# Kernel optimization log

Hardware: AMD Instinct MI355X
Metric: run time of the kernel (lower is better)

Reference implementation:

```python
import jax, jax.numpy as jnp
import numpy as np

N = 32000
E = 512000
IN_C = 16
OUT_C = 16
EDGE_DIM = 8
HID = 32


def setup_inputs() -> dict:
    key = jax.random.key(0)
    ks = jax.random.split(key, 8)
    x = jax.random.normal(ks[0], (N, IN_C), dtype=jnp.float32)
    edge_index = jax.random.randint(ks[1], (2, E), 0, N, dtype=jnp.int32)
    pseudo = jax.random.uniform(ks[2], (E, EDGE_DIM), dtype=jnp.float32)
    W1 = jax.random.normal(ks[3], (EDGE_DIM, HID), dtype=jnp.float32) * (1.0 / np.sqrt(EDGE_DIM))
    b1 = jnp.zeros((HID,), dtype=jnp.float32)
    W2 = jax.random.normal(ks[4], (HID, IN_C * OUT_C), dtype=jnp.float32) * (1.0 / np.sqrt(HID))
    b2 = jnp.zeros((IN_C * OUT_C,), dtype=jnp.float32)
    root = jax.random.normal(ks[5], (IN_C, OUT_C), dtype=jnp.float32) * (1.0 / np.sqrt(IN_C))
    bias = jnp.zeros((OUT_C,), dtype=jnp.float32)
    return {"x": x, "edge_index": edge_index, "pseudo": pseudo,
            "W1": W1, "b1": b1, "W2": W2, "b2": b2,
            "root": root, "bias": bias}


def reference(x, edge_index, pseudo, W1, b1, W2, b2, root, bias):
    row, col = edge_index[0], edge_index[1]
    # edge MLP h_Theta: [E, edge_dim] -> [E, in*out]
    h = jax.nn.relu(pseudo @ W1 + b1)
    w = (h @ W2 + b2).reshape(-1, IN_C, OUT_C)  # [E, in, out]
    # gather source features, per-edge matmul: [E, in] x [E, in, out] -> [E, out]
    msg = jnp.einsum('ei,eio->eo', x[col], w)
    # scatter-add messages to destination nodes (aggr='add')
    out = jax.ops.segment_sum(msg, row, num_segments=N)
    # root transform + bias
    out = out + x @ root + bias
    return out
```

## Files before the change

kernel.cpp:

```cpp
#include <hip/hip_runtime.h>
#include <stdint.h>
#include <limits.h>

#define IN_C   16
#define OUT_C  16
#define EDGE_DIM 8
#define HID    32
#define HSTR   20
#define XSTR   20
#define MAXDEG 48
#define FEPB   128

typedef __attribute__((ext_vector_type(8))) short short8v;
typedef __attribute__((ext_vector_type(4))) float f32x4;

__device__ __forceinline__ uint32_t pack_bf16(float a, float b) {
    union { float f; uint32_t u; } ua, ub;
    ua.f = a; ub.f = b;
    uint32_t lo = (ua.u + 0x7FFFu + ((ua.u >> 16) & 1u)) >> 16;
    uint32_t hi = (ub.u + 0x7FFFu + ((ub.u >> 16) & 1u)) >> 16;
    return (lo & 0xFFFFu) | (hi << 16);
}

__global__ __launch_bounds__(256) void nnconv_prep(
    const float* __restrict__ W2, uint4* __restrict__ W2p,
    int* __restrict__ zero_base, int n_zero_ints)
{
    int bid = blockIdx.x;
    if (bid < 4) {
        int idx = bid * 256 + threadIdx.x;
        int ci = idx >> 6, l = idx & 63;
        int o = l & 15, g = l >> 4;
        uint32_t u[4];
        #pragma unroll
        for (int v = 0; v < 4; ++v) {
            int k0 = g * 8 + 2 * v;
            u[v] = pack_bf16(W2[(size_t)k0 * 256 + ci * 16 + o],
                             W2[(size_t)(k0 + 1) * 256 + ci * 16 + o]);
        }
        W2p[idx] = make_uint4(u[0], u[1], u[2], u[3]);
        return;
    }
    int t = (bid - 4) * 256 + threadIdx.x;
    int stride = (gridDim.x - 4) * 256;
    for (int i = t; i < n_zero_ints; i += stride)
        zero_base[i] = 0;
}

__global__ __launch_bounds__(256, 2) void nnconv_fused1(
    const float* __restrict__ pseudo, const int* __restrict__ eidx,
    const float* __restrict__ x,
    const float* __restrict__ W1, const float* __restrict__ b1,
    const uint4* __restrict__ W2p, const float* __restrict__ b2,
    int* __restrict__ cur, float* __restrict__ ovf,
    float* __restrict__ msg, int n_edges)
{
    __shared__ uint32_t Hl[FEPB * HSTR];
    __shared__ float    xl[FEPB * XSTR];
    __shared__ uint4    Wl[1024];

    int t  = threadIdx.x;
    int e0 = blockIdx.x * FEPB;
    int e  = e0 + t;
    bool valid = e < n_edges;
    int lane = t & 63, w = t >> 6;
    int o = lane & 15, g = lane >> 4;

    int row = 0;
    float p[EDGE_DIM];
    {
        float4* xd = reinterpret_cast<float4*>(&xl[t * XSTR]);
        if (valid) {
            row = eidx[e];
            int c = eidx[n_edges + e];
            const float4* xp = reinterpret_cast<const float4*>(x + (size_t)c * IN_C);
            xd[0] = xp[0]; xd[1] = xp[1]; xd[2] = xp[2]; xd[3] = xp[3];
            const float4* pp = reinterpret_cast<const float4*>(pseudo + (size_t)e * EDGE_DIM);
            float4 p0 = pp[0], p1 = pp[1];
            p[0]=p0.x; p[1]=p0.y; p[2]=p0.z; p[3]=p0.w;
            p[4]=p1.x; p[5]=p1.y; p[6]=p1.z; p[7]=p1.w;
        } else {
            float4 z = make_float4(0.f, 0.f, 0.f, 0.f);
            xd[0] = z; xd[1] = z; xd[2] = z; xd[3] = z;
            #pragma unroll
            for (int k = 0; k < EDGE_DIM; ++k) p[k] = 0.f;
        }
    }
    float b2v[16];
    #pragma unroll
    for (int ci = 0; ci < 16; ++ci) b2v[ci] = b2[ci * 16 + o];

    for (int ch = 0; ch < 4; ++ch) {
        uint4 c0 = W2p[lane + (ch * 4 + 0) * 64];
        uint4 c1 = W2p[lane + (ch * 4 + 1) * 64];
        uint4 c2 = W2p[lane + (ch * 4 + 2) * 64];
        uint4 c3 = W2p[lane + (ch * 4 + 3) * 64];
        Wl[lane + (ch * 4 + 0) * 64] = c0;
        Wl[lane + (ch * 4 + 1) * 64] = c1;
        Wl[lane + (ch * 4 + 2) * 64] = c2;
        Wl[lane + (ch * 4 + 3) * 64] = c3;
    }

    {
        float h[HID];
        #pragma unroll
        for (int j = 0; j < HID; ++j) h[j] = b1[j];
        #pragma unroll
        for (int k = 0; k < EDGE_DIM; ++k) {
            float pk = p[k];
            const float* wr = W1 + k * HID;
            #pragma unroll
            for (int j = 0; j < HID; ++j)
                h[j] = fmaf(pk, wr[j], h[j]);
        }
        uint32_t hw[16];
        #pragma unroll
        for (int v = 0; v < 16; ++v) {
            float a0 = h[2*v]   > 0.f ? h[2*v]   : 0.f;
            float a1 = h[2*v+1] > 0.f ? h[2*v+1] : 0.f;
            hw[v] = valid ? pack_bf16(a0, a1) : 0u;
        }
        uint4* hp = reinterpret_cast<uint4*>(&Hl[t * HSTR]);
        hp[0] = make_uint4(hw[0],  hw[1],  hw[2],  hw[3]);
        hp[1] = make_uint4(hw[4],  hw[5],  hw[6],  hw[7]);
        hp[2] = make_uint4(hw[8],  hw[9],  hw[10], hw[11]);
        hp[3] = make_uint4(hw[12], hw[13], hw[14], hw[15]);
    }

    int slv = INT_MIN;
    if (valid) {
        int rank = atomicAdd(&cur[row], 1);
        slv = (rank < MAXDEG) ? (row * MAXDEG + rank) : (-row - 1);
    }

    int ebase = w * 64;

    #pragma unroll
    for (int q = 0; q < 4; ++q) {
        short8v A = *reinterpret_cast<const short8v*>(
            &Hl[(size_t)(ebase + q * 16 + o) * HSTR + g * 4]);
        float macc[4] = {0.f, 0.f, 0.f, 0.f};
        #pragma unroll
        for (int cq = 0; cq < 4; ++cq) {
            short8v Bf[4];
            #pragma unroll
            for (int j = 0; j < 4; ++j)
                Bf[j] = *reinterpret_cast<const short8v*>(&Wl[(cq * 4 + j) * 64 + lane]);
            f32x4 C[4];
            #pragma unroll
            for (int j = 0; j < 4; ++j) {
                float bb = b2v[cq * 4 + j];
                C[j] = __builtin_amdgcn_mfma_f32_16x16x32_bf16(
                    A, Bf[j], (f32x4){bb, bb, bb, bb}, 0, 0, 0);
            }
            #pragma unroll
            for (int r = 0; r < 4; ++r) {
                int el = ebase + q * 16 + g * 4 + r;
                float4 xa = *reinterpret_cast<const float4*>(&xl[el * XSTR + cq * 4]);
                float m = macc[r];
                m = fmaf(xa.x, C[0][r], m); m = fmaf(xa.y, C[1][r], m);
                m = fmaf(xa.z, C[2][r], m); m = fmaf(xa.w, C[3][r], m);
                macc[r] = m;
            }
        }
        #pragma unroll
        for (int r = 0; r < 4; ++r) {
            int el = q * 16 + g * 4 + r;
            int sl = __shfl(slv, el, 64);
            if (sl >= 0)
                msg[(size_t)sl * OUT_C + o] = macc[r];
            else if (sl != INT_MIN)
                atomicAdd(&ovf[(size_t)(-sl - 1) * OUT_C + o], macc[r]);
        }
    }
}

__global__ __launch_bounds__(256) void nnconv_gather1(
    const float* __restrict__ msg, const int* __restrict__ cur,
    const float* __restrict__ ovf, const float* __restrict__ x,
    const float* __restrict__ root, const float* __restrict__ bias,
    float* __restrict__ out, int n_nodes)
{
    int wave = threadIdx.x >> 6, lane = threadIdx.x & 63;
    int n = blockIdx.x * 4 + wave;
    if (n >= n_nodes) return;
    int group = lane >> 4, o = lane & 15;
    int cntn = cur[n]; if (cntn > MAXDEG) cntn = MAXDEG;
    size_t s = (size_t)n * MAXDEG;
    float acc = 0.f;
    for (int k = group; k < cntn; k += 4)
        acc += msg[(s + k) * OUT_C + o];
    acc += __shfl_xor(acc, 16, 64);
    acc += __shfl_xor(acc, 32, 64);
    if (group == 0) {
        float r = bias[o] + ovf[(size_t)n * OUT_C + o];
        const float* xr = x + (size_t)n * IN_C;
        #pragma unroll
        for (int i = 0; i < IN_C; ++i)
            r = fmaf(xr[i], root[i * OUT_C + o], r);
        out[n * OUT_C + o] = r + acc;
    }
}


__global__ __launch_bounds__(256) void nnconv_init_out(
    const float* __restrict__ x, const float* __restrict__ root,
    const float* __restrict__ bias, float* __restrict__ out, int n_nodes)
{
    int t = blockIdx.x * blockDim.x + threadIdx.x;
    if (t >= n_nodes * OUT_C) return;
    int n = t >> 4, o = t & 15;
    float acc = bias[o];
    #pragma unroll
    for (int i = 0; i < IN_C; ++i)
        acc = fmaf(x[n * IN_C + i], root[i * OUT_C + o], acc);
    out[t] = acc;
}

__global__ __launch_bounds__(256) void nnconv_edge_atomic(
    const float* __restrict__ x, const int* __restrict__ edge_index,
    const float* __restrict__ pseudo,
    const float* __restrict__ W1, const float* __restrict__ b1,
    const float* __restrict__ W2, const float* __restrict__ b2,
    float* __restrict__ out, int n_edges)
{
    int e = blockIdx.x * blockDim.x + threadIdx.x;
    if (e >= n_edges) return;
    int row = edge_index[e];
    int col = edge_index[n_edges + e];
    float p[EDGE_DIM];
    const float4* pp = reinterpret_cast<const float4*>(pseudo + (size_t)e * EDGE_DIM);
    float4 p0 = pp[0], p1 = pp[1];
    p[0]=p0.x; p[1]=p0.y; p[2]=p0.z; p[3]=p0.w;
    p[4]=p1.x; p[5]=p1.y; p[6]=p1.z; p[7]=p1.w;
    float h[HID];
    #pragma unroll
    for (int j = 0; j < HID; ++j) {
        float a = b1[j];
        #pragma unroll
        for (int k = 0; k < EDGE_DIM; ++k)
            a = fmaf(p[k], W1[k * HID + j], a);
        h[j] = a > 0.f ? a : 0.f;
    }
    float xg[IN_C];
    const float4* xp = reinterpret_cast<const float4*>(x + (size_t)col * IN_C);
    #pragma unroll
    for (int q = 0; q < 4; ++q) {
        float4 v = xp[q];
        xg[q*4+0]=v.x; xg[q*4+1]=v.y; xg[q*4+2]=v.z; xg[q*4+3]=v.w;
    }
    float m[OUT_C];
    #pragma unroll
    for (int o = 0; o < OUT_C; ++o) m[o] = 0.f;
    for (int i = 0; i < IN_C; ++i) {
        float wv[OUT_C];
        const float* b2r = b2 + i * OUT_C;
        #pragma unroll
        for (int o = 0; o < OUT_C; ++o) wv[o] = b2r[o];
        #pragma unroll
        for (int j = 0; j < HID; ++j) {
            float hj = h[j];
            const float* wr = W2 + j * (IN_C * OUT_C) + i * OUT_C;
            #pragma unroll
            for (int o = 0; o < OUT_C; ++o)
                wv[o] = fmaf(hj, wr[o], wv[o]);
        }
        float xi = xg[i];
        #pragma unroll
        for (int o = 0; o < OUT_C; ++o)
            m[o] = fmaf(xi, wv[o], m[o]);
    }
    float* op = out + (size_t)row * OUT_C;
    #pragma unroll
    for (int o = 0; o < OUT_C; ++o)
        atomicAdd(op + o, m[o]);
}


extern "C" void kernel_launch(void* const* d_in, const int* in_sizes, int n_in,
                              void* d_out, int out_size, void* d_ws, size_t ws_size,
                              hipStream_t stream) {
    const float* x      = (const float*)d_in[0];
    const int*   eidx   = (const int*)  d_in[1];
    const float* pseudo = (const float*)d_in[2];
    const float* W1     = (const float*)d_in[3];
    const float* b1     = (const float*)d_in[4];
    const float* W2     = (const float*)d_in[5];
    const float* b2     = (const float*)d_in[6];
    const float* root   = (const float*)d_in[7];
    const float* bias   = (const float*)d_in[8];
    float* out = (float*)d_out;

    int n_nodes = in_sizes[0] / IN_C;
    int n_edges = in_sizes[1] / 2;
    int eblocks256 = (n_edges + 255) / 256;
    char* wsp = (char*)d_ws;

    {
        int* cur1  = (int*)wsp;
        float* ovf = (float*)(cur1 + n_nodes);
        size_t off = sizeof(int) * (size_t)n_nodes + sizeof(float) * (size_t)n_nodes * OUT_C;
        off = (off + 255) & ~(size_t)255;
        uint4* W2p = (uint4*)(wsp + off);
        off += sizeof(uint4) * 1024;
        off = (off + 255) & ~(size_t)255;
        float* msg = (float*)(wsp + off);
        size_t need = off + sizeof(float) * (size_t)n_nodes * MAXDEG * OUT_C;

        if (ws_size >= need) {
            int n_zero_ints = n_nodes + n_nodes * OUT_C;
            nnconv_prep<<<4 + 64, 256, 0, stream>>>(W2, W2p, cur1, n_zero_ints);
            nnconv_fused1<<<(n_edges + FEPB - 1) / FEPB, FEPB, 0, stream>>>(
                pseudo, eidx, x, W1, b1, W2p, b2, cur1, ovf, msg, n_edges);
            nnconv_gather1<<<(n_nodes + 3) / 4, 256, 0, stream>>>(
                msg, cur1, ovf, x, root, bias, out, n_nodes);
            return;
        }
    }

    nnconv_init_out<<<(n_nodes * OUT_C + 255) / 256, 256, 0, stream>>>(
        x, root, bias, out, n_nodes);
    nnconv_edge_atomic<<<eblocks256, 256, 0, stream>>>(
        x, eidx, pseudo, W1, b1, W2, b2, out, n_edges);
}
```

Measured before the change: 76.40 us.

## Store per-edge messages as packed bf16 and skip overflow reads

Per-edge messages written to the slotted staging buffer are now packed into bf16 pairs, using a lane shuffle to bring neighbouring outputs together. This halves the bytes written by the fused edge kernel and read back by the gather kernel. The gather only reads the overflow accumulator when the node's degree exceeds the slot capacity, and b2 is pre-transposed so it can be loaded with vector loads. Rounding messages to bf16 before summation costs accuracy.

```diff
diff --git a/kernel.cpp b/kernel.cpp
--- a/kernel.cpp
+++ b/kernel.cpp
@@ -24,6 +24,7 @@
 
 __global__ __launch_bounds__(256) void nnconv_prep(
     const float* __restrict__ W2, uint4* __restrict__ W2p,
+    const float* __restrict__ b2, float* __restrict__ b2t,
     int* __restrict__ zero_base, int n_zero_ints)
 {
     int bid = blockIdx.x;
@@ -41,8 +42,13 @@
         W2p[idx] = make_uint4(u[0], u[1], u[2], u[3]);
         return;
     }
-    int t = (bid - 4) * 256 + threadIdx.x;
-    int stride = (gridDim.x - 4) * 256;
+    if (bid == 4) {
+        int t = threadIdx.x;
+        b2t[t] = b2[(t & 15) * 16 + (t >> 4)];
+        return;
+    }
+    int t = (bid - 5) * 256 + threadIdx.x;
+    int stride = (gridDim.x - 5) * 256;
     for (int i = t; i < n_zero_ints; i += stride)
         zero_base[i] = 0;
 }
@@ -51,9 +57,9 @@
     const float* __restrict__ pseudo, const int* __restrict__ eidx,
     const float* __restrict__ x,
     const float* __restrict__ W1, const float* __restrict__ b1,
-    const uint4* __restrict__ W2p, const float* __restrict__ b2,
+    const uint4* __restrict__ W2p, const float* __restrict__ b2t,
     int* __restrict__ cur, float* __restrict__ ovf,
-    float* __restrict__ msg, int n_edges)
+    uint32_t* __restrict__ msgu, int n_edges)
 {
     __shared__ uint32_t Hl[FEPB * HSTR];
     __shared__ float    xl[FEPB * XSTR];
@@ -87,8 +93,15 @@
         }
     }
     float b2v[16];
-    #pragma unroll
-    for (int ci = 0; ci < 16; ++ci) b2v[ci] = b2[ci * 16 + o];
+    {
+        const float4* bp = reinterpret_cast<const float4*>(b2t + o * 16);
+        #pragma unroll
+        for (int c4 = 0; c4 < 4; ++c4) {
+            float4 bv = bp[c4];
+            b2v[c4*4+0] = bv.x; b2v[c4*4+1] = bv.y;
+            b2v[c4*4+2] = bv.z; b2v[c4*4+3] = bv.w;
+        }
+    }
 
     for (int ch = 0; ch < 4; ++ch) {
         uint4 c0 = W2p[lane + (ch * 4 + 0) * 64];
@@ -167,16 +180,21 @@
         for (int r = 0; r < 4; ++r) {
             int el = q * 16 + g * 4 + r;
             int sl = __shfl(slv, el, 64);
-            if (sl >= 0)
-                msg[(size_t)sl * OUT_C + o] = macc[r];
-            else if (sl != INT_MIN)
+            float other = __shfl_xor(macc[r], 1, 64);
+            if (sl >= 0) {
+                if (!(o & 1)) {
+                    uint32_t dw = pack_bf16(macc[r], other);
+                    msgu[(size_t)sl * 8 + (o >> 1)] = dw;
+                }
+            } else if (sl != INT_MIN) {
                 atomicAdd(&ovf[(size_t)(-sl - 1) * OUT_C + o], macc[r]);
+            }
         }
     }
 }
 
 __global__ __launch_bounds__(256) void nnconv_gather1(
-    const float* __restrict__ msg, const int* __restrict__ cur,
+    const uint32_t* __restrict__ msgu, const int* __restrict__ cur,
     const float* __restrict__ ovf, const float* __restrict__ x,
     const float* __restrict__ root, const float* __restrict__ bias,
     float* __restrict__ out, int n_nodes)
@@ -185,15 +203,23 @@
     int n = blockIdx.x * 4 + wave;
     if (n >= n_nodes) return;
     int group = lane >> 4, o = lane & 15;
-    int cntn = cur[n]; if (cntn > MAXDEG) cntn = MAXDEG;
+    int craw = cur[n];
+    int cntn = craw > MAXDEG ? MAXDEG : craw;
     size_t s = (size_t)n * MAXDEG;
     float acc = 0.f;
-    for (int k = group; k < cntn; k += 4)
-        acc += msg[(s + k) * OUT_C + o];
+    int half = o & 1;
+    int dwi = o >> 1;
+    for (int k = group; k < cntn; k += 4) {
+        uint32_t u = msgu[(s + k) * 8 + dwi];
+        uint32_t h16 = half ? (u & 0xFFFF0000u) : (u << 16);
+        union { uint32_t u; float f; } cv; cv.u = h16;
+        acc += cv.f;
+    }
     acc += __shfl_xor(acc, 16, 64);
     acc += __shfl_xor(acc, 32, 64);
     if (group == 0) {
-        float r = bias[o] + ovf[(size_t)n * OUT_C + o];
+        float r = bias[o];
+        if (craw > MAXDEG) r += ovf[(size_t)n * OUT_C + o];
         const float* xr = x + (size_t)n * IN_C;
         #pragma unroll
         for (int i = 0; i < IN_C; ++i)
@@ -303,17 +329,19 @@
         off = (off + 255) & ~(size_t)255;
         uint4* W2p = (uint4*)(wsp + off);
         off += sizeof(uint4) * 1024;
+        float* b2t = (float*)(wsp + off);
+        off += sizeof(float) * 256;
         off = (off + 255) & ~(size_t)255;
-        float* msg = (float*)(wsp + off);
-        size_t need = off + sizeof(float) * (size_t)n_nodes * MAXDEG * OUT_C;
+        uint32_t* msgu = (uint32_t*)(wsp + off);
+        size_t need = off + sizeof(uint32_t) * (size_t)n_nodes * MAXDEG * 8;
 
         if (ws_size >= need) {
             int n_zero_ints = n_nodes + n_nodes * OUT_C;
-            nnconv_prep<<<4 + 64, 256, 0, stream>>>(W2, W2p, cur1, n_zero_ints);
+            nnconv_prep<<<5 + 64, 256, 0, stream>>>(W2, W2p, b2, b2t, cur1, n_zero_ints);
             nnconv_fused1<<<(n_edges + FEPB - 1) / FEPB, FEPB, 0, stream>>>(
-                pseudo, eidx, x, W1, b1, W2p, b2, cur1, ovf, msg, n_edges);
+                pseudo, eidx, x, W1, b1, W2p, b2t, cur1, ovf, msgu, n_edges);
             nnconv_gather1<<<(n_nodes + 3) / 4, 256, 0, stream>>>(
-                msg, cur1, ovf, x, root, bias, out, n_nodes);
+                msgu, cur1, ovf, x, root, bias, out, n_nodes);
             return;
         }
     }
```

Result: slower. 78.82 us (+3.2%).
